# Kernel optimization log

Measured on AMD Instinct MI355X. Metric: run time of the kernel, lower is better.

## Reference

```python
import jax, jax.numpy as jnp
import numpy as np

B, S, H, E, F, TOP_K = 4, 2048, 512, 16, 1024, 2


def setup_inputs() -> dict:
    key = jax.random.key(0)
    k0, k1, k2, k3, k4 = jax.random.split(key, 5)
    scale = 0.02
    return {
        "inputs": jax.random.normal(k0, (B, S, H), dtype=jnp.float32),
        "router_w": jax.random.normal(k1, (E, H), dtype=jnp.float32) * scale,
        "gate_w": jax.random.normal(k2, (E, H, F), dtype=jnp.float32) * scale,
        "up_w": jax.random.normal(k3, (E, H, F), dtype=jnp.float32) * scale,
        "down_w": jax.random.normal(k4, (E, F, H), dtype=jnp.float32) * scale,
    }


def _moe_forward(inputs, router_w, gate_w, up_w, down_w):
    b, s, h = inputs.shape
    x = inputs.reshape(-1, h)                      # [T, H]
    T = x.shape[0]
    # --- routing: topk of logits then fp32 softmax over the k selected ---
    router_logits = x @ router_w.T                 # [T, E]
    top_vals, top_idx = jax.lax.top_k(router_logits, TOP_K)   # [T, K]
    weights = jax.nn.softmax(top_vals.astype(jnp.float32), axis=-1)  # [T, K]
    # dense combine weights: w[t, e] = routing weight if expert e selected else 0
    combine = jnp.zeros((T, router_w.shape[0]), jnp.float32)
    combine = combine.at[jnp.arange(T)[:, None], top_idx].set(weights)  # [T, E]

    # --- per-expert SwiGLU MLP, weighted combine (scan over experts) ---
    def step(acc, ew):
        wg, wu, wd, ce = ew                        # [H,F], [H,F], [F,H], [T]
        hid = jax.nn.silu(x @ wg) * (x @ wu)       # [T, F]
        y = hid @ wd                               # [T, H]
        return acc + ce[:, None] * y, None

    out0 = jnp.zeros_like(x)
    out, _ = jax.lax.scan(step, out0, (gate_w, up_w, down_w, combine.T))
    return out.reshape(b, s, h), router_logits, top_idx


def reference(inputs, router_w, gate_w, up_w, down_w):
    out, router_logits, selected_experts = _moe_forward(
        inputs, router_w, gate_w, up_w, down_w)
    return out
```

## Files before the change

kernel.cpp:

```cpp
#include <hip/hip_runtime.h>
#include <cstdint>
#include <cstddef>

#define T_TOK 8192
#define H_DIM 512
#define E_NUM 16
#define F_DIM 1024

typedef __bf16 bf16x8 __attribute__((ext_vector_type(8)));
typedef float f32x4 __attribute__((ext_vector_type(4)));

#define OFF_XBF  0UL
#define OFF_HID  8388608UL
#define OFF_GW   41943040UL
#define OFF_UW   58720256UL
#define OFF_DW   75497472UL
#define OFF_STOK 92274688UL
#define OFF_SW   92340224UL
#define OFF_TOPE 92405760UL
#define OFF_TOPW 92471296UL
#define OFF_CNT  92536832UL
#define OFF_CUR  92537856UL
#define OFF_OFFS 92538880UL
#define OFF_SIDX 92539904UL
#define OFF_YB   OFF_GW

__device__ __forceinline__ unsigned short f2bf(float f) {
  union { float f; uint32_t u; } v; v.f = f;
  uint32_t r = v.u + 0x7fffu + ((v.u >> 16) & 1u);
  return (unsigned short)(r >> 16);
}

__device__ __forceinline__ float bf2f(unsigned short u) {
  union { uint32_t u; float f; } v; v.u = (uint32_t)u << 16;
  return v.f;
}

__device__ __forceinline__ void gld16(const void* g, void* l) {
  __builtin_amdgcn_global_load_lds(
      (const __attribute__((address_space(1))) unsigned int*)g,
      (__attribute__((address_space(3))) unsigned int*)l, 16, 0, 0);
}

__global__ __launch_bounds__(256) void k_pre(
    const float* __restrict__ x, const float* __restrict__ rw,
    const float* __restrict__ gw, const float* __restrict__ uw,
    const float* __restrict__ dw,
    unsigned short* __restrict__ xbf, int* __restrict__ tope,
    float* __restrict__ topw,
    unsigned short* __restrict__ gws, unsigned short* __restrict__ uws,
    unsigned short* __restrict__ dws) {
  const int bid = blockIdx.x;
  const int tid = threadIdx.x;
  __shared__ float ls[32 * 260];

  if (bid < 4096) {
    const int fx = bid & 7, kc = (bid >> 3) & 15, ez = bid >> 7;
    const int e = ez >> 1;
    const float* src = ((ez & 1) ? uw : gw) + (size_t)e * H_DIM * F_DIM;
    unsigned short* dst = ((ez & 1) ? uws : gws);
    #pragma unroll
    for (int j = 0; j < 4; ++j) {
      int vi = tid + j * 256;
      int row = vi >> 5, c4 = (vi & 31) * 4;
      float4 v = *(const float4*)&src[(size_t)(kc*32 + row) * F_DIM + fx*128 + c4];
      ls[row*132 + c4+0]=v.x; ls[row*132 + c4+1]=v.y;
      ls[row*132 + c4+2]=v.z; ls[row*132 + c4+3]=v.w;
    }
    __syncthreads();
    size_t obase = (((size_t)e * 8 + fx) * 16 + kc) * 4096;
    #pragma unroll
    for (int j = 0; j < 2; ++j) {
      int oi = tid + j * 256;
      int f = oi >> 2, slot = oi & 3;
      int ks = ((slot ^ f) & 3) * 8;
      uint4 o;
      o.x = (uint32_t)f2bf(ls[(ks+0)*132 + f]) | ((uint32_t)f2bf(ls[(ks+1)*132 + f]) << 16);
      o.y = (uint32_t)f2bf(ls[(ks+2)*132 + f]) | ((uint32_t)f2bf(ls[(ks+3)*132 + f]) << 16);
      o.z = (uint32_t)f2bf(ls[(ks+4)*132 + f]) | ((uint32_t)f2bf(ls[(ks+5)*132 + f]) << 16);
      o.w = (uint32_t)f2bf(ls[(ks+6)*132 + f]) | ((uint32_t)f2bf(ls[(ks+7)*132 + f]) << 16);
      *(uint4*)&dst[obase + (size_t)oi * 8] = o;
    }
  } else if (bid < 5120) {
    const int i = bid - 4096;
    const int ht = i & 1, kc = (i >> 1) & 31, e = i >> 6;
    const float* src = dw + (size_t)e * F_DIM * H_DIM;
    #pragma unroll
    for (int j = 0; j < 8; ++j) {
      int vi = tid + j * 256;
      int row = vi >> 6, c4 = (vi & 63) * 4;
      float4 v = *(const float4*)&src[(size_t)(kc*32 + row) * H_DIM + ht*256 + c4];
      ls[row*260 + c4+0]=v.x; ls[row*260 + c4+1]=v.y;
      ls[row*260 + c4+2]=v.z; ls[row*260 + c4+3]=v.w;
    }
    __syncthreads();
    size_t obase = (((size_t)e * 2 + ht) * 32 + kc) * 8192;
    #pragma unroll
    for (int j = 0; j < 4; ++j) {
      int oi = tid + j * 256;
      int h = oi >> 2, slot = oi & 3;
      int ks = ((slot ^ h) & 3) * 8;
      uint4 o;
      o.x = (uint32_t)f2bf(ls[(ks+0)*260 + h]) | ((uint32_t)f2bf(ls[(ks+1)*260 + h]) << 16);
      o.y = (uint32_t)f2bf(ls[(ks+2)*260 + h]) | ((uint32_t)f2bf(ls[(ks+3)*260 + h]) << 16);
      o.z = (uint32_t)f2bf(ls[(ks+4)*260 + h]) | ((uint32_t)f2bf(ls[(ks+5)*260 + h]) << 16);
      o.w = (uint32_t)f2bf(ls[(ks+6)*260 + h]) | ((uint32_t)f2bf(ls[(ks+7)*260 + h]) << 16);
      *(uint4*)&dws[obase + (size_t)oi * 8] = o;
    }
  } else {
    const int rb = bid - 5120;
    const int wave = tid >> 6, lane = tid & 63;
    const int t = rb * 4 + wave;
    const float4* xr = (const float4*)(x + (size_t)t * H_DIM + lane * 8);
    float4 a = xr[0], b = xr[1];
    float xi[8] = {a.x, a.y, a.z, a.w, b.x, b.y, b.z, b.w};
    uint4 o;
    o.x = (uint32_t)f2bf(xi[0]) | ((uint32_t)f2bf(xi[1]) << 16);
    o.y = (uint32_t)f2bf(xi[2]) | ((uint32_t)f2bf(xi[3]) << 16);
    o.z = (uint32_t)f2bf(xi[4]) | ((uint32_t)f2bf(xi[5]) << 16);
    o.w = (uint32_t)f2bf(xi[6]) | ((uint32_t)f2bf(xi[7]) << 16);
    *(uint4*)(xbf + (size_t)t * H_DIM + lane * 8) = o;
    float acc[E_NUM];
    #pragma unroll
    for (int e = 0; e < E_NUM; ++e) {
      const float4* wr = (const float4*)(rw + e * H_DIM + lane * 8);
      float4 wa = wr[0], wb = wr[1];
      acc[e] = xi[0]*wa.x + xi[1]*wa.y + xi[2]*wa.z + xi[3]*wa.w
             + xi[4]*wb.x + xi[5]*wb.y + xi[6]*wb.z + xi[7]*wb.w;
    }
    #pragma unroll
    for (int off = 1; off < 64; off <<= 1) {
      #pragma unroll
      for (int e = 0; e < E_NUM; ++e) acc[e] += __shfl_xor(acc[e], off);
    }
    if (lane == 0) {
      int e0 = 0; float v0 = acc[0];
      #pragma unroll
      for (int e = 1; e < E_NUM; ++e) if (acc[e] > v0) { v0 = acc[e]; e0 = e; }
      int e1 = -1; float v1 = -3.4e38f;
      #pragma unroll
      for (int e = 0; e < E_NUM; ++e) if (e != e0 && acc[e] > v1) { v1 = acc[e]; e1 = e; }
      float ee = __expf(v1 - v0);
      float inv = 1.0f / (1.0f + ee);
      tope[t*2]   = e0; tope[t*2+1] = e1;
      topw[t*2]   = inv; topw[t*2+1] = ee * inv;
    }
  }
}

__global__ __launch_bounds__(256) void k_hist(
    const int* __restrict__ tope, int* __restrict__ counts) {
  __shared__ int lh[E_NUM];
  const int tid = threadIdx.x;
  if (tid < E_NUM) lh[tid] = 0;
  __syncthreads();
  atomicAdd(&lh[tope[blockIdx.x * 256 + tid]], 1);
  __syncthreads();
  if (tid < E_NUM) atomicAdd(&counts[tid * 16], lh[tid]);
}

__global__ void k_offsets(const int* __restrict__ counts, int* __restrict__ offs) {
  if (threadIdx.x == 0 && blockIdx.x == 0) {
    int s = 0;
    for (int e = 0; e < E_NUM; ++e) { offs[e] = s; s += counts[e * 16]; }
    offs[E_NUM] = s;
  }
}

__global__ __launch_bounds__(256) void k_scatter(
    const int* __restrict__ tope, const float* __restrict__ topw,
    const int* __restrict__ offs, int* __restrict__ cursors,
    int* __restrict__ stok, float* __restrict__ sw, int* __restrict__ sidx) {
  __shared__ int lh[E_NUM];
  __shared__ int lbase[E_NUM];
  const int tid = threadIdx.x;
  const int t = blockIdx.x * 256 + tid;
  if (tid < E_NUM) lh[tid] = 0;
  __syncthreads();
  int e0 = tope[t*2], e1 = tope[t*2+1];
  int r0 = atomicAdd(&lh[e0], 1);
  int r1 = atomicAdd(&lh[e1], 1);
  __syncthreads();
  if (tid < E_NUM) lbase[tid] = atomicAdd(&cursors[tid * 16], lh[tid]);
  __syncthreads();
  int s0 = offs[e0] + lbase[e0] + r0;
  int s1 = offs[e1] + lbase[e1] + r1;
  stok[s0] = t; sw[s0] = topw[t*2];
  stok[s1] = t; sw[s1] = topw[t*2+1];
  sidx[t*2] = s0; sidx[t*2+1] = s1;
}

__global__ __launch_bounds__(256, 2) void k_gateup(
    const unsigned short* __restrict__ xbf,
    const unsigned short* __restrict__ gws, const unsigned short* __restrict__ uws,
    const int* __restrict__ stok, const int* __restrict__ counts,
    const int* __restrict__ offs, unsigned short* __restrict__ hid) {
  const int e = blockIdx.z;
  const int cnt = counts[e * 16];
  const int t0 = blockIdx.y * 128;
  if (t0 >= cnt) return;
  const int base = offs[e];
  const int fx = blockIdx.x;

  __shared__ __align__(16) unsigned short sb[2][3][4096];

  const int tid = threadIdx.x;
  const int wave = tid >> 6, lane = tid & 63;
  const int l15 = lane & 15, hi = lane >> 4;
  const int wm = wave >> 1, wn = wave & 1;

  const int r0 = tid >> 2, slot = tid & 3;
  const int rr0 = min(t0 + r0, cnt - 1), rr1 = min(t0 + r0 + 64, cnt - 1);
  const char* sA0 = (const char*)xbf + (size_t)stok[base + rr0] * 1024 + ((slot ^ (r0 & 3)) * 16);
  const char* sA1 = (const char*)xbf + (size_t)stok[base + rr1] * 1024 + ((slot ^ (r0 & 3)) * 16);
  const char* sG = (const char*)gws + (((size_t)e * 8 + fx) * 16) * 8192 + tid * 16;
  const char* sU = (const char*)uws + (((size_t)e * 8 + fx) * 16) * 8192 + tid * 16;
  unsigned short* const dA = &sb[0][0][wave * 512];
  unsigned short* const dG = &sb[0][1][wave * 512];
  unsigned short* const dU = &sb[0][2][wave * 512];
  const int bufo = 3 * 4096;

  f32x4 accg[4][4] = {}; f32x4 accu[4][4] = {};

  #define STAGE_GU(b, kk) { \
    gld16(sA0 + (kk)*64, dA + (b)*bufo); \
    gld16(sA1 + (kk)*64, dA + (b)*bufo + 2048); \
    gld16(sG + (size_t)(kk)*8192, dG + (b)*bufo); \
    gld16(sG + (size_t)(kk)*8192 + 4096, dG + (b)*bufo + 2048); \
    gld16(sU + (size_t)(kk)*8192, dU + (b)*bufo); \
    gld16(sU + (size_t)(kk)*8192 + 4096, dU + (b)*bufo + 2048); }

  STAGE_GU(0, 0);
  __syncthreads();
  #pragma unroll 1
  for (int kk = 0; kk < 16; ++kk) {
    const int cur = kk & 1;
    if (kk < 15) STAGE_GU(cur ^ 1, kk + 1);
    const unsigned short* lA = &sb[cur][0][0];
    const unsigned short* lG = &sb[cur][1][0];
    const unsigned short* lU = &sb[cur][2][0];
    bf16x8 a[4], bg[4], bu[4];
    #pragma unroll
    for (int m = 0; m < 4; ++m) {
      int row = wm*64 + m*16 + l15;
      a[m] = *(const bf16x8*)((const char*)lA + row*64 + (((hi ^ row) & 3) << 4));
    }
    #pragma unroll
    for (int s = 0; s < 4; ++s) {
      int row = wn*64 + s*16 + l15;
      int o = row*64 + (((hi ^ row) & 3) << 4);
      bg[s] = *(const bf16x8*)((const char*)lG + o);
      bu[s] = *(const bf16x8*)((const char*)lU + o);
    }
    #pragma unroll
    for (int m = 0; m < 4; ++m)
      #pragma unroll
      for (int s = 0; s < 4; ++s) {
        accg[m][s] = __builtin_amdgcn_mfma_f32_16x16x32_bf16(a[m], bg[s], accg[m][s], 0, 0, 0);
        accu[m][s] = __builtin_amdgcn_mfma_f32_16x16x32_bf16(a[m], bu[s], accu[m][s], 0, 0, 0);
      }
    __syncthreads();
  }
  #undef STAGE_GU

  #pragma unroll
  for (int m = 0; m < 4; ++m)
    #pragma unroll
    for (int r = 0; r < 4; ++r) {
      int row = t0 + wm*64 + m*16 + hi*4 + r;
      if (row < cnt) {
        #pragma unroll
        for (int s = 0; s < 4; ++s) {
          float g = accg[m][s][r], u = accu[m][s][r];
          float h = g / (1.0f + __expf(-g)) * u;
          hid[(size_t)(base + row) * 1024 + fx*128 + wn*64 + s*16 + l15] = f2bf(h);
        }
      }
    }
}

__global__ __launch_bounds__(256, 3) void k_down(
    const unsigned short* __restrict__ hid, const unsigned short* __restrict__ dws,
    const int* __restrict__ counts, const int* __restrict__ offs,
    unsigned short* __restrict__ ybuf) {
  const int e = blockIdx.z;
  const int cnt = counts[e * 16];
  const int t0 = blockIdx.y * 64;
  if (t0 >= cnt) return;
  const int base = offs[e];
  const int ht = blockIdx.x;

  __shared__ __align__(16) unsigned short sbA[2][2048];
  __shared__ __align__(16) unsigned short sbW[2][8192];

  const int tid = threadIdx.x;
  const int wave = tid >> 6, lane = tid & 63;
  const int l15 = lane & 15, hi = lane >> 4;

  const int r0 = tid >> 2, slot = tid & 3;
  const int rr = min(t0 + r0, cnt - 1);
  const char* sA = (const char*)hid + (size_t)(base + rr) * 2048 + ((slot ^ (r0 & 3)) * 16);
  const char* sW = (const char*)dws + (((size_t)e * 2 + ht) * 32) * 16384 + tid * 16;
  unsigned short* const dA = &sbA[0][wave * 512];
  unsigned short* const dW = &sbW[0][wave * 512];

  f32x4 acc[4][4] = {};

  #define STAGE_DN(b, kk) { \
    gld16(sA + (kk)*64, dA + (b)*2048); \
    const char* w = sW + (size_t)(kk)*16384; \
    gld16(w,         dW + (b)*8192); \
    gld16(w + 4096,  dW + (b)*8192 + 2048); \
    gld16(w + 8192,  dW + (b)*8192 + 4096); \
    gld16(w + 12288, dW + (b)*8192 + 6144); }

  STAGE_DN(0, 0);
  __syncthreads();
  #pragma unroll 1
  for (int kk = 0; kk < 32; ++kk) {
    const int cur = kk & 1;
    if (kk < 31) STAGE_DN(cur ^ 1, kk + 1);
    const unsigned short* lA = &sbA[cur][0];
    const unsigned short* lW = &sbW[cur][0];
    bf16x8 a[4], b[4];
    #pragma unroll
    for (int m = 0; m < 4; ++m) {
      int row = m*16 + l15;
      a[m] = *(const bf16x8*)((const char*)lA + row*64 + (((hi ^ row) & 3) << 4));
    }
    #pragma unroll
    for (int s = 0; s < 4; ++s) {
      int row = wave*64 + s*16 + l15;
      b[s] = *(const bf16x8*)((const char*)lW + row*64 + (((hi ^ row) & 3) << 4));
    }
    #pragma unroll
    for (int m = 0; m < 4; ++m)
      #pragma unroll
      for (int s = 0; s < 4; ++s)
        acc[m][s] = __builtin_amdgcn_mfma_f32_16x16x32_bf16(a[m], b[s], acc[m][s], 0, 0, 0);
    __syncthreads();
  }
  #undef STAGE_DN

  #pragma unroll
  for (int m = 0; m < 4; ++m)
    #pragma unroll
    for (int r = 0; r < 4; ++r) {
      int row = t0 + m*16 + hi*4 + r;
      if (row < cnt) {
        unsigned short* y = ybuf + (size_t)(base + row) * 512 + ht*256 + wave*64;
        #pragma unroll
        for (int s = 0; s < 4; ++s)
          y[s*16 + l15] = f2bf(acc[m][s][r]);
      }
    }
}

__global__ __launch_bounds__(256) void k_gather(
    const unsigned short* __restrict__ ybuf, const int* __restrict__ sidx,
    const float* __restrict__ topw, float* __restrict__ out) {
  const int wave = threadIdx.x >> 6, lane = threadIdx.x & 63;
  const int t = blockIdx.x * 4 + wave;
  const int s0 = sidx[t*2], s1 = sidx[t*2+1];
  const float w0 = topw[t*2], w1 = topw[t*2+1];
  uint4 a = *(const uint4*)(ybuf + (size_t)s0 * 512 + lane * 8);
  uint4 b = *(const uint4*)(ybuf + (size_t)s1 * 512 + lane * 8);
  float4 o0, o1;
  o0.x = w0*bf2f((unsigned short)(a.x)) + w1*bf2f((unsigned short)(b.x));
  o0.y = w0*bf2f((unsigned short)(a.x>>16)) + w1*bf2f((unsigned short)(b.x>>16));
  o0.z = w0*bf2f((unsigned short)(a.y)) + w1*bf2f((unsigned short)(b.y));
  o0.w = w0*bf2f((unsigned short)(a.y>>16)) + w1*bf2f((unsigned short)(b.y>>16));
  o1.x = w0*bf2f((unsigned short)(a.z)) + w1*bf2f((unsigned short)(b.z));
  o1.y = w0*bf2f((unsigned short)(a.z>>16)) + w1*bf2f((unsigned short)(b.z>>16));
  o1.z = w0*bf2f((unsigned short)(a.w)) + w1*bf2f((unsigned short)(b.w));
  o1.w = w0*bf2f((unsigned short)(a.w>>16)) + w1*bf2f((unsigned short)(b.w>>16));
  float* orow = out + (size_t)t * H_DIM + lane * 8;
  *(float4*)orow = o0;
  *(float4*)(orow + 4) = o1;
}

extern "C" void kernel_launch(void* const* d_in, const int* in_sizes, int n_in,
                              void* d_out, int out_size, void* d_ws, size_t ws_size,
                              hipStream_t stream) {
  const float* x  = (const float*)d_in[0];
  const float* rw = (const float*)d_in[1];
  const float* gw = (const float*)d_in[2];
  const float* uw = (const float*)d_in[3];
  const float* dw = (const float*)d_in[4];
  float* out = (float*)d_out;
  char* ws = (char*)d_ws;

  unsigned short* xbf = (unsigned short*)(ws + OFF_XBF);
  unsigned short* hid = (unsigned short*)(ws + OFF_HID);
  unsigned short* gws = (unsigned short*)(ws + OFF_GW);
  unsigned short* uws = (unsigned short*)(ws + OFF_UW);
  unsigned short* dws = (unsigned short*)(ws + OFF_DW);
  unsigned short* ybuf = (unsigned short*)(ws + OFF_YB);
  int*   stok    = (int*)(ws + OFF_STOK);
  float* swt     = (float*)(ws + OFF_SW);
  int*   tope    = (int*)(ws + OFF_TOPE);
  float* topw    = (float*)(ws + OFF_TOPW);
  int*   counts  = (int*)(ws + OFF_CNT);
  int*   cursors = (int*)(ws + OFF_CUR);
  int*   offs    = (int*)(ws + OFF_OFFS);
  int*   sidx    = (int*)(ws + OFF_SIDX);

  hipMemsetAsync(ws + OFF_CNT, 0, 2048 + 128, stream);

  k_pre<<<7168, 256, 0, stream>>>(x, rw, gw, uw, dw, xbf, tope, topw, gws, uws, dws);
  k_hist<<<T_TOK * 2 / 256, 256, 0, stream>>>(tope, counts);
  k_offsets<<<1, 64, 0, stream>>>(counts, offs);
  k_scatter<<<T_TOK / 256, 256, 0, stream>>>(tope, topw, offs, cursors, stok, swt, sidx);
  k_gateup<<<dim3(8, T_TOK * 2 / 128, E_NUM), 256, 0, stream>>>(
      xbf, gws, uws, stok, counts, offs, hid);
  k_down<<<dim3(2, T_TOK * 2 / 64, E_NUM), 256, 0, stream>>>(
      hid, dws, counts, offs, ybuf);
  k_gather<<<T_TOK / 4, 256, 0, stream>>>(ybuf, sidx, topw, out);
}
```

Measured before the change: 158.1 us.

## Compact expert tile lists for grouped GEMM grids and rework weight conversion

Builds compact per-tile work lists (expert, token offset) in k_offsets so k_gateup and k_down launch a dense grid of at most 160/288 rows instead of a 16x-oversized 3D grid with mostly early-exiting blocks. The weight transpose/convert in k_pre is also restructured: each thread loads 8 rows of float4, converts to bf16 before writing to LDS, and handles larger tiles, so fewer blocks are launched and LDS traffic is halved. The fixed grid sizes assume the tile counts never exceed the bounds, which holds because total assignments are T*2.

```diff
diff --git a/kernel.cpp b/kernel.cpp
--- a/kernel.cpp
+++ b/kernel.cpp
@@ -23,6 +23,8 @@
 #define OFF_CUR  92537856UL
 #define OFF_OFFS 92538880UL
 #define OFF_SIDX 92539904UL
+#define OFF_L128 92605440UL
+#define OFF_L64  92606464UL
 #define OFF_YB   OFF_GW
 
 __device__ __forceinline__ unsigned short f2bf(float f) {
@@ -52,63 +54,69 @@
     unsigned short* __restrict__ dws) {
   const int bid = blockIdx.x;
   const int tid = threadIdx.x;
-  __shared__ float ls[32 * 260];
-
-  if (bid < 4096) {
-    const int fx = bid & 7, kc = (bid >> 3) & 15, ez = bid >> 7;
-    const int e = ez >> 1;
-    const float* src = ((ez & 1) ? uw : gw) + (size_t)e * H_DIM * F_DIM;
-    unsigned short* dst = ((ez & 1) ? uws : gws);
-    #pragma unroll
-    for (int j = 0; j < 4; ++j) {
-      int vi = tid + j * 256;
-      int row = vi >> 5, c4 = (vi & 31) * 4;
-      float4 v = *(const float4*)&src[(size_t)(kc*32 + row) * F_DIM + fx*128 + c4];
-      ls[row*132 + c4+0]=v.x; ls[row*132 + c4+1]=v.y;
-      ls[row*132 + c4+2]=v.z; ls[row*132 + c4+3]=v.w;
+  __shared__ __align__(16) uint32_t lsu[4096];
+
+  if (bid < 3072) {
+    const int isgu = (bid < 2048);
+    const float* src;
+    unsigned short* dst;
+    size_t obase0;
+    int ldn;
+    int e, kc;
+    if (isgu) {
+      e = bid >> 7;
+      const int mat = (bid >> 6) & 1;
+      kc = (bid >> 2) & 15;
+      const int f2 = bid & 3;
+      src = (mat ? uw : gw) + (size_t)e * H_DIM * F_DIM + (size_t)kc * 32 * F_DIM + f2 * 256;
+      dst = mat ? uws : gws;
+      obase0 = (((size_t)e * 8 + f2 * 2) * 16 + kc) * 4096;
+      ldn = F_DIM;
+    } else {
+      const int r = bid - 2048;
+      e = r >> 6;
+      kc = (r >> 1) & 31;
+      const int ht = r & 1;
+      src = dw + (size_t)e * F_DIM * H_DIM + (size_t)kc * 32 * H_DIM + ht * 256;
+      dst = dws;
+      obase0 = (((size_t)e * 2 + ht) * 32 + kc) * 8192;
+      ldn = H_DIM;
+    }
+    const int nb = tid & 63, kb = tid >> 6;
+    const float* s0 = src + (size_t)kb * 8 * ldn + nb * 4;
+    float4 v[8];
+    #pragma unroll
+    for (int j = 0; j < 8; ++j) v[j] = *(const float4*)(s0 + (size_t)j * ldn);
+    #pragma unroll
+    for (int i = 0; i < 4; ++i) {
+      const int n = nb * 4 + i;
+      uint4 q;
+      q.x = (uint32_t)f2bf(((const float*)&v[0])[i]) | ((uint32_t)f2bf(((const float*)&v[1])[i]) << 16);
+      q.y = (uint32_t)f2bf(((const float*)&v[2])[i]) | ((uint32_t)f2bf(((const float*)&v[3])[i]) << 16);
+      q.z = (uint32_t)f2bf(((const float*)&v[4])[i]) | ((uint32_t)f2bf(((const float*)&v[5])[i]) << 16);
+      q.w = (uint32_t)f2bf(((const float*)&v[6])[i]) | ((uint32_t)f2bf(((const float*)&v[7])[i]) << 16);
+      const int jr = n >> 1, sw = (jr ^ (jr >> 3)) & 7;
+      const int ccs = (((n & 1) << 2) + kb) ^ sw;
+      *(uint4*)&lsu[jr * 32 + ccs * 4] = q;
     }
     __syncthreads();
-    size_t obase = (((size_t)e * 8 + fx) * 16 + kc) * 4096;
-    #pragma unroll
-    for (int j = 0; j < 2; ++j) {
-      int oi = tid + j * 256;
-      int f = oi >> 2, slot = oi & 3;
-      int ks = ((slot ^ f) & 3) * 8;
-      uint4 o;
-      o.x = (uint32_t)f2bf(ls[(ks+0)*132 + f]) | ((uint32_t)f2bf(ls[(ks+1)*132 + f]) << 16);
-      o.y = (uint32_t)f2bf(ls[(ks+2)*132 + f]) | ((uint32_t)f2bf(ls[(ks+3)*132 + f]) << 16);
-      o.z = (uint32_t)f2bf(ls[(ks+4)*132 + f]) | ((uint32_t)f2bf(ls[(ks+5)*132 + f]) << 16);
-      o.w = (uint32_t)f2bf(ls[(ks+6)*132 + f]) | ((uint32_t)f2bf(ls[(ks+7)*132 + f]) << 16);
-      *(uint4*)&dst[obase + (size_t)oi * 8] = o;
-    }
-  } else if (bid < 5120) {
-    const int i = bid - 4096;
-    const int ht = i & 1, kc = (i >> 1) & 31, e = i >> 6;
-    const float* src = dw + (size_t)e * F_DIM * H_DIM;
-    #pragma unroll
-    for (int j = 0; j < 8; ++j) {
-      int vi = tid + j * 256;
-      int row = vi >> 6, c4 = (vi & 63) * 4;
-      float4 v = *(const float4*)&src[(size_t)(kc*32 + row) * H_DIM + ht*256 + c4];
-      ls[row*260 + c4+0]=v.x; ls[row*260 + c4+1]=v.y;
-      ls[row*260 + c4+2]=v.z; ls[row*260 + c4+3]=v.w;
-    }
-    __syncthreads();
-    size_t obase = (((size_t)e * 2 + ht) * 32 + kc) * 8192;
-    #pragma unroll
-    for (int j = 0; j < 4; ++j) {
-      int oi = tid + j * 256;
-      int h = oi >> 2, slot = oi & 3;
-      int ks = ((slot ^ h) & 3) * 8;
-      uint4 o;
-      o.x = (uint32_t)f2bf(ls[(ks+0)*260 + h]) | ((uint32_t)f2bf(ls[(ks+1)*260 + h]) << 16);
-      o.y = (uint32_t)f2bf(ls[(ks+2)*260 + h]) | ((uint32_t)f2bf(ls[(ks+3)*260 + h]) << 16);
-      o.z = (uint32_t)f2bf(ls[(ks+4)*260 + h]) | ((uint32_t)f2bf(ls[(ks+5)*260 + h]) << 16);
-      o.w = (uint32_t)f2bf(ls[(ks+6)*260 + h]) | ((uint32_t)f2bf(ls[(ks+7)*260 + h]) << 16);
-      *(uint4*)&dws[obase + (size_t)oi * 8] = o;
+    const int n = tid;
+    const int jr = n >> 1, sw = (jr ^ (jr >> 3)) & 7;
+    #pragma unroll
+    for (int c = 0; c < 4; ++c) {
+      const int ccs = (((n & 1) << 2) + c) ^ sw;
+      uint4 q = *(const uint4*)&lsu[jr * 32 + ccs * 4];
+      if (isgu) {
+        const int fi = n & 127, s = (c ^ fi) & 3;
+        const size_t ob = obase0 + (size_t)(n >> 7) * 16 * 4096;
+        *(uint4*)&dst[ob + fi * 32 + s * 8] = q;
+      } else {
+        const int s = (c ^ n) & 3;
+        *(uint4*)&dst[obase0 + n * 32 + s * 8] = q;
+      }
     }
   } else {
-    const int rb = bid - 5120;
+    const int rb = bid - 3072;
     const int wave = tid >> 6, lane = tid & 63;
     const int t = rb * 4 + wave;
     const float4* xr = (const float4*)(x + (size_t)t * H_DIM + lane * 8);
@@ -159,11 +167,25 @@
   if (tid < E_NUM) atomicAdd(&counts[tid * 16], lh[tid]);
 }
 
-__global__ void k_offsets(const int* __restrict__ counts, int* __restrict__ offs) {
-  if (threadIdx.x == 0 && blockIdx.x == 0) {
-    int s = 0;
-    for (int e = 0; e < E_NUM; ++e) { offs[e] = s; s += counts[e * 16]; }
-    offs[E_NUM] = s;
+__global__ void k_offsets(const int* __restrict__ counts, int* __restrict__ offs,
+                          int* __restrict__ list128, int* __restrict__ list64) {
+  __shared__ int sc[16], b128[16], b64[16];
+  if (threadIdx.x == 0) {
+    int s = 0, a = 0, b = 0;
+    for (int e = 0; e < E_NUM; ++e) {
+      int c = counts[e * 16];
+      sc[e] = c; b128[e] = a; b64[e] = b;
+      offs[e] = s;
+      s += c; a += (c + 127) >> 7; b += (c + 63) >> 6;
+    }
+    offs[16] = s; offs[18] = a; offs[19] = b;
+  }
+  __syncthreads();
+  for (int e = 0; e < E_NUM; ++e) {
+    const int n1 = (sc[e] + 127) >> 7;
+    for (int ti = threadIdx.x; ti < n1; ti += 64) list128[b128[e] + ti] = (e << 24) | (ti << 7);
+    const int n2 = (sc[e] + 63) >> 6;
+    for (int ti = threadIdx.x; ti < n2; ti += 64) list64[b64[e] + ti] = (e << 24) | (ti << 6);
   }
 }
 
@@ -194,11 +216,13 @@
     const unsigned short* __restrict__ xbf,
     const unsigned short* __restrict__ gws, const unsigned short* __restrict__ uws,
     const int* __restrict__ stok, const int* __restrict__ counts,
-    const int* __restrict__ offs, unsigned short* __restrict__ hid) {
-  const int e = blockIdx.z;
+    const int* __restrict__ offs, const int* __restrict__ list128,
+    unsigned short* __restrict__ hid) {
+  const int y = blockIdx.y;
+  if (y >= offs[18]) return;
+  const int v = list128[y];
+  const int e = v >> 24, t0 = v & 0xffffff;
   const int cnt = counts[e * 16];
-  const int t0 = blockIdx.y * 128;
-  if (t0 >= cnt) return;
   const int base = offs[e];
   const int fx = blockIdx.x;
 
@@ -282,11 +306,12 @@
 __global__ __launch_bounds__(256, 3) void k_down(
     const unsigned short* __restrict__ hid, const unsigned short* __restrict__ dws,
     const int* __restrict__ counts, const int* __restrict__ offs,
-    unsigned short* __restrict__ ybuf) {
-  const int e = blockIdx.z;
+    const int* __restrict__ list64, unsigned short* __restrict__ ybuf) {
+  const int y = blockIdx.y;
+  if (y >= offs[19]) return;
+  const int v = list64[y];
+  const int e = v >> 24, t0 = v & 0xffffff;
   const int cnt = counts[e * 16];
-  const int t0 = blockIdx.y * 64;
-  if (t0 >= cnt) return;
   const int base = offs[e];
   const int ht = blockIdx.x;
 
@@ -348,10 +373,10 @@
     for (int r = 0; r < 4; ++r) {
       int row = t0 + m*16 + hi*4 + r;
       if (row < cnt) {
-        unsigned short* y = ybuf + (size_t)(base + row) * 512 + ht*256 + wave*64;
+        unsigned short* yy = ybuf + (size_t)(base + row) * 512 + ht*256 + wave*64;
         #pragma unroll
         for (int s = 0; s < 4; ++s)
-          y[s*16 + l15] = f2bf(acc[m][s][r]);
+          yy[s*16 + l15] = f2bf(acc[m][s][r]);
       }
     }
 }
@@ -404,16 +429,18 @@
   int*   cursors = (int*)(ws + OFF_CUR);
   int*   offs    = (int*)(ws + OFF_OFFS);
   int*   sidx    = (int*)(ws + OFF_SIDX);
+  int*   list128 = (int*)(ws + OFF_L128);
+  int*   list64  = (int*)(ws + OFF_L64);
 
   hipMemsetAsync(ws + OFF_CNT, 0, 2048 + 128, stream);
 
-  k_pre<<<7168, 256, 0, stream>>>(x, rw, gw, uw, dw, xbf, tope, topw, gws, uws, dws);
+  k_pre<<<5120, 256, 0, stream>>>(x, rw, gw, uw, dw, xbf, tope, topw, gws, uws, dws);
   k_hist<<<T_TOK * 2 / 256, 256, 0, stream>>>(tope, counts);
-  k_offsets<<<1, 64, 0, stream>>>(counts, offs);
+  k_offsets<<<1, 64, 0, stream>>>(counts, offs, list128, list64);
   k_scatter<<<T_TOK / 256, 256, 0, stream>>>(tope, topw, offs, cursors, stok, swt, sidx);
-  k_gateup<<<dim3(8, T_TOK * 2 / 128, E_NUM), 256, 0, stream>>>(
-      xbf, gws, uws, stok, counts, offs, hid);
-  k_down<<<dim3(2, T_TOK * 2 / 64, E_NUM), 256, 0, stream>>>(
-      hid, dws, counts, offs, ybuf);
+  k_gateup<<<dim3(8, 160), 256, 0, stream>>>(
+      xbf, gws, uws, stok, counts, offs, list128, hid);
+  k_down<<<dim3(2, 288), 256, 0, stream>>>(
+      hid, dws, counts, offs, list64, ybuf);
   k_gather<<<T_TOK / 4, 256, 0, stream>>>(ybuf, sidx, topw, out);
 }
```

After: 153.9 us. 2.7% less time.
